# Optimization experiments

Hardware: AMD Instinct MI355X
Metric: run time of the kernel (lower is better)

The kernel has to match this reference:

```python
import jax, jax.numpy as jnp
import numpy as np

B, T, IN_DIM, EMB = 8, 2048, 1024, 1024
NEG_INF = -1e30  # stand-in for float('-inf'); exp() underflows to 0 identically


def setup_inputs() -> dict:
    key = jax.random.key(0)
    ks = jax.random.split(key, 7)
    s = 1.0 / np.sqrt(IN_DIM)
    return {
        "x": jax.random.normal(ks[0], (B, T, IN_DIM), dtype=jnp.float32),
        "Wq": jax.random.normal(ks[1], (IN_DIM, EMB), dtype=jnp.float32) * s,
        "bq": jax.random.normal(ks[2], (EMB,), dtype=jnp.float32) * 0.01,
        "Wk": jax.random.normal(ks[3], (IN_DIM, EMB), dtype=jnp.float32) * s,
        "bk": jax.random.normal(ks[4], (EMB,), dtype=jnp.float32) * 0.01,
        "Wv": jax.random.normal(ks[5], (IN_DIM, EMB), dtype=jnp.float32) * s,
        "bv": jax.random.normal(ks[6], (EMB,), dtype=jnp.float32) * 0.01,
    }


def reference(x, Wq, bq, Wk, bk, Wv, bv):
    # projections: [B, T, EMB]
    q = x @ Wq + bq
    k = x @ Wk + bk
    v = x @ Wv + bv
    scale = jnp.asarray(EMB, x.dtype) ** 0.5
    # scores: [B, T, T]
    scores = jnp.einsum("btd,bsd->bts", q, k) / scale
    Tq = scores.shape[-2]
    causal = jnp.tril(jnp.ones((Tq, Tq), dtype=bool))  # [T, T]
    scores = jnp.where(causal, scores, jnp.asarray(NEG_INF, scores.dtype))
    # Faithful to torch.vmap(softmax): per-batch GLOBAL-matrix softmax
    # (max and sum taken over the whole [T, T] matrix, not per row).
    m = jnp.max(scores, axis=(-2, -1), keepdims=True)
    e = jnp.exp(scores - m)
    w = e / jnp.sum(e, axis=(-2, -1), keepdims=True)
    # output: [B, T, EMB]
    return jnp.einsum("bts,bsd->btd", w, v)
```

## Files before the change

### kernel.cpp

```cpp
#include <hip/hip_runtime.h>
#include <stdint.h>


#define B_   8
#define T_   2048
#define DIM  1024

typedef _Float16 f16;
typedef f16   f16x8 __attribute__((ext_vector_type(8)));
typedef f16   f16x4 __attribute__((ext_vector_type(4)));
typedef float f32x4 __attribute__((ext_vector_type(4)));

typedef const __attribute__((address_space(1))) void gvoid_t;
typedef __attribute__((address_space(3))) void lvoid_t;

__device__ __forceinline__ void stage_half256(const uint16_t* __restrict__ g, int ld,
                                              uint16_t* s, int tid) {
#pragma unroll
  for (int j = 0; j < 2; ++j) {
    int r   = j * 64 + (tid >> 3);
    int seg = (tid & 7) ^ (r & 7);
    const uint16_t* gp = g + (size_t)r * ld + seg * 8;
    uint16_t* sp = s + j * 4096 + (tid >> 6) * 512;
    __builtin_amdgcn_global_load_lds((gvoid_t*)gp, (lvoid_t*)sp, 16, 0, 0);
  }
}

__device__ __forceinline__ f16x8 frag64(const uint16_t* s, int r, int gseg) {
  return *(const f16x8*)(s + r * 64 + ((gseg ^ (r & 7)) * 8));
}

__device__ __forceinline__ void stage_u8k(const uint16_t* __restrict__ g, int ld,
                                          uint16_t* s, int tid) {
  int r   = tid >> 2;
  int seg = (tid & 3) ^ (r & 3);
  const uint16_t* gp = g + (size_t)r * ld + seg * 8;
  uint16_t* sp = s + (tid >> 6) * 512;
  __builtin_amdgcn_global_load_lds((gvoid_t*)gp, (lvoid_t*)sp, 16, 0, 0);
}

__device__ __forceinline__ f16x8 frag32(const uint16_t* s, int r, int gseg) {
  return *(const f16x8*)(s + r * 32 + ((gseg ^ (r & 3)) * 8));
}

__device__ __forceinline__ void lda4(const uint16_t* s, int rbase, int quad, int l15,
                                     f16x8 o[4][2]) {
#pragma unroll
  for (int mf = 0; mf < 4; ++mf) {
    int r = rbase + mf * 16 + l15;
#pragma unroll
    for (int kk = 0; kk < 2; ++kk) o[mf][kk] = frag64(s, r, kk * 4 + quad);
  }
}

__device__ __forceinline__ void ldb1(const uint16_t* s, int rbase, int quad, int l15,
                                     f16x8 o[2]) {
  int r = rbase + l15;
#pragma unroll
  for (int kk = 0; kk < 2; ++kk) o[kk] = frag64(s, r, kk * 4 + quad);
}

__device__ __forceinline__ void lda4q(const uint16_t* s, int rbase, int quad, int l15,
                                      f16x8 o[4]) {
#pragma unroll
  for (int mf = 0; mf < 4; ++mf) o[mf] = frag32(s, rbase + mf * 16 + l15, quad);
}

__device__ __forceinline__ void ldb2q(const uint16_t* s, int rbase, int quad, int l15,
                                      f16x8 o[2]) {
#pragma unroll
  for (int nf = 0; nf < 2; ++nf) o[nf] = frag32(s, rbase + nf * 16 + l15, quad);
}

template <int M0, int N0>
__device__ __forceinline__ void mm8(f16x8 a[4][2], f16x8 b[2], f32x4 (&acc)[8][2]) {
#pragma unroll
  for (int kk = 0; kk < 2; ++kk)
#pragma unroll
    for (int mf = 0; mf < 4; ++mf)
      acc[M0 + mf][N0] = __builtin_amdgcn_mfma_f32_16x16x32_f16(
          a[mf][kk], b[kk], acc[M0 + mf][N0], 0, 0, 0);
}

template <int N0>
__device__ __forceinline__ void mm8q(f16x8 a[4], f16x8 b[2], f32x4 (&acc)[4][4]) {
#pragma unroll
  for (int mf = 0; mf < 4; ++mf)
#pragma unroll
    for (int nf = 0; nf < 2; ++nf)
      acc[mf][N0 + nf] = __builtin_amdgcn_mfma_f32_16x16x32_f16(
          a[mf], b[nf], acc[mf][N0 + nf], 0, 0, 0);
}

#define SYNC_MFMA8(AA, BB, M0, N0)                     \
  __builtin_amdgcn_s_barrier();                        \
  asm volatile("s_waitcnt lgkmcnt(0)" ::: "memory");   \
  __builtin_amdgcn_s_setprio(1);                       \
  mm8<M0, N0>(AA, BB, acc);                            \
  __builtin_amdgcn_s_setprio(0);                       \
  __builtin_amdgcn_s_barrier();

#define SYNC_MFMA8Q(AA, BB, N0)                        \
  __builtin_amdgcn_s_barrier();                        \
  asm volatile("s_waitcnt lgkmcnt(0)" ::: "memory");   \
  __builtin_amdgcn_s_setprio(1);                       \
  mm8q<N0>(AA, BB, acc);                               \
  __builtin_amdgcn_s_setprio(0);                       \
  __builtin_amdgcn_s_barrier();

__device__ __forceinline__ void gemm128x256_bk32(const uint16_t* __restrict__ gA,
                                                 const uint16_t* __restrict__ gB,
                                                 int lda, int ldb, int nTiles,
                                                 uint16_t* smem, f32x4 (&acc)[4][4]) {
  const int tid = threadIdx.x, lane = tid & 63;
  const int quad = lane >> 4, l15 = lane & 15;
  const int wv = tid >> 6, wr = wv >> 2, wc = wv & 3;

  uint16_t* sA0 = smem;
  uint16_t* sA1 = smem + 4096;
  uint16_t* sB0 = smem + 8192;
  uint16_t* sB1 = smem + 16384;

  stage_u8k(gA,                          lda, sA0,        tid);
  stage_u8k(gB,                          ldb, sB0,        tid);
  stage_u8k(gB + 128 * (size_t)ldb,      ldb, sB0 + 4096, tid);
  stage_u8k(gA + 32,                     lda, sA1,        tid);
  asm volatile("s_waitcnt vmcnt(1)" ::: "memory");
  __builtin_amdgcn_s_barrier();

  f16x8 a[4], b0[2], b1[2];
#pragma unroll 1
  for (int it = 0; it < nTiles / 2 - 1; ++it) {
    const uint16_t* gAn = gA + (2 * it + 2) * 32;
    const uint16_t* gBn = gB + (2 * it + 1) * 32;
    lda4q(sA0, wr * 64,      quad, l15, a);
    ldb2q(sB0, wc * 64,      quad, l15, b0);
    stage_u8k(gBn,                     ldb, sB1,        tid);
    stage_u8k(gBn + 128 * (size_t)ldb, ldb, sB1 + 4096, tid);
    SYNC_MFMA8Q(a, b0, 0)
    ldb2q(sB0, wc * 64 + 32, quad, l15, b1);
    stage_u8k(gAn, lda, sA0, tid);
    asm volatile("s_waitcnt vmcnt(1)" ::: "memory");
    SYNC_MFMA8Q(a, b1, 2)
    lda4q(sA1, wr * 64,      quad, l15, a);
    ldb2q(sB1, wc * 64,      quad, l15, b0);
    stage_u8k(gBn + 32,                     ldb, sB0,        tid);
    stage_u8k(gBn + 32 + 128 * (size_t)ldb, ldb, sB0 + 4096, tid);
    SYNC_MFMA8Q(a, b0, 0)
    ldb2q(sB1, wc * 64 + 32, quad, l15, b1);
    stage_u8k(gAn + 32, lda, sA1, tid);
    asm volatile("s_waitcnt vmcnt(1)" ::: "memory");
    SYNC_MFMA8Q(a, b1, 2)
  }
  {
    const uint16_t* gBn = gB + (nTiles - 1) * 32;
    lda4q(sA0, wr * 64,      quad, l15, a);
    ldb2q(sB0, wc * 64,      quad, l15, b0);
    stage_u8k(gBn,                     ldb, sB1,        tid);
    stage_u8k(gBn + 128 * (size_t)ldb, ldb, sB1 + 4096, tid);
    SYNC_MFMA8Q(a, b0, 0)
    ldb2q(sB0, wc * 64 + 32, quad, l15, b1);
    asm volatile("s_waitcnt vmcnt(0)" ::: "memory");
    SYNC_MFMA8Q(a, b1, 2)
    lda4q(sA1, wr * 64,      quad, l15, a);
    ldb2q(sB1, wc * 64,      quad, l15, b0);
    SYNC_MFMA8Q(a, b0, 0)
    ldb2q(sB1, wc * 64 + 32, quad, l15, b1);
    SYNC_MFMA8Q(a, b1, 2)
  }
}

__device__ __forceinline__ void gemm256n128_8ph(const uint16_t* __restrict__ gA,
                                                const uint16_t* __restrict__ gB,
                                                int lda, int ldb, int nIter,
                                                uint16_t* smem, f32x4 (&acc)[8][2]) {
  const int tid = threadIdx.x, lane = tid & 63;
  const int quad = lane >> 4, l15 = lane & 15;
  const int wv = tid >> 6, wr = wv >> 2, wc = wv & 3;

  uint16_t* sA0 = smem;
  uint16_t* sA1 = smem + 16384;
  uint16_t* sB0 = smem + 32768;
  uint16_t* sB1 = smem + 40960;

  stage_half256(gA,                     lda, sA0,        tid);
  stage_half256(gA + 128 * (size_t)lda, lda, sA0 + 8192, tid);
  stage_half256(gB,                     ldb, sB0,        tid);
  stage_half256(gB + 64,                ldb, sB1,        tid);
  asm volatile("s_waitcnt vmcnt(2)" ::: "memory");
  __builtin_amdgcn_s_barrier();

  f16x8 alo[4][2], ahi[4][2], b0[2], b1[2];
#pragma unroll 1
  for (int it = 0; it < nIter - 1; ++it) {
    const int t1 = 2 * it + 1, t2 = 2 * it + 2, t3 = 2 * it + 3;
    const uint16_t* gA1 = gA + t1 * 64;
    const uint16_t* gA2 = gA + t2 * 64;

    lda4(sA0, wr * 128,      quad, l15, alo);
    ldb1(sB0, wc * 32,       quad, l15, b0);
    stage_half256(gA1, lda, sA1, tid);
    SYNC_MFMA8(alo, b0, 0, 0)
    ldb1(sB0, wc * 32 + 16,  quad, l15, b1);
    stage_half256(gA1 + 128 * (size_t)lda, lda, sA1 + 8192, tid);
    SYNC_MFMA8(alo, b1, 0, 1)
    lda4(sA0, wr * 128 + 64, quad, l15, ahi);
    stage_half256(gB + t2 * 64, ldb, sB0, tid);
    SYNC_MFMA8(ahi, b1, 4, 1)
    asm volatile("s_waitcnt vmcnt(2)" ::: "memory");
    SYNC_MFMA8(ahi, b0, 4, 0)
    lda4(sA1, wr * 128,      quad, l15, alo);
    ldb1(sB1, wc * 32,       quad, l15, b0);
    stage_half256(gA2, lda, sA0, tid);
    SYNC_MFMA8(alo, b0, 0, 0)
    ldb1(sB1, wc * 32 + 16,  quad, l15, b1);
    stage_half256(gA2 + 128 * (size_t)lda, lda, sA0 + 8192, tid);
    SYNC_MFMA8(alo, b1, 0, 1)
    lda4(sA1, wr * 128 + 64, quad, l15, ahi);
    stage_half256(gB + t3 * 64, ldb, sB1, tid);
    SYNC_MFMA8(ahi, b1, 4, 1)
    asm volatile("s_waitcnt vmcnt(2)" ::: "memory");
    SYNC_MFMA8(ahi, b0, 4, 0)
  }
  {
    const uint16_t* gA1 = gA + (2 * nIter - 1) * 64;
    lda4(sA0, wr * 128,      quad, l15, alo);
    ldb1(sB0, wc * 32,       quad, l15, b0);
    stage_half256(gA1, lda, sA1, tid);
    SYNC_MFMA8(alo, b0, 0, 0)
    ldb1(sB0, wc * 32 + 16,  quad, l15, b1);
    stage_half256(gA1 + 128 * (size_t)lda, lda, sA1 + 8192, tid);
    SYNC_MFMA8(alo, b1, 0, 1)
    lda4(sA0, wr * 128 + 64, quad, l15, ahi);
    SYNC_MFMA8(ahi, b1, 4, 1)
    asm volatile("s_waitcnt vmcnt(0)" ::: "memory");
    SYNC_MFMA8(ahi, b0, 4, 0)
    lda4(sA1, wr * 128,      quad, l15, alo);
    ldb1(sB1, wc * 32,       quad, l15, b0);
    SYNC_MFMA8(alo, b0, 0, 0)
    ldb1(sB1, wc * 32 + 16,  quad, l15, b1);
    SYNC_MFMA8(alo, b1, 0, 1)
    lda4(sA1, wr * 128 + 64, quad, l15, ahi);
    SYNC_MFMA8(ahi, b1, 4, 1)
    SYNC_MFMA8(ahi, b0, 4, 0)
  }
}


__global__ void zero_lrow_kernel(float* __restrict__ lrow) {
  lrow[blockIdx.x * 256 + threadIdx.x] = 0.f;
}

__global__ void conv_x_kernel(const float* __restrict__ x, f16* __restrict__ xf) {
  size_t i = (size_t)blockIdx.x * 256 + threadIdx.x;
  float4 v = ((const float4*)x)[i];
  f16x4 o = {(f16)v.x, (f16)v.y, (f16)v.z, (f16)v.w};
  ((f16x4*)xf)[i] = o;
}

__global__ void convT_w_kernel(const float* __restrict__ Wq, const float* __restrict__ Wk,
                               const float* __restrict__ Wv, f16* __restrict__ WT) {
  __shared__ float tile[64][65];
  const int z = blockIdx.z;
  const float* W = (z == 0) ? Wq : (z == 1) ? Wk : Wv;
  const int r0 = blockIdx.x * 64, c0 = blockIdx.y * 64, tid = threadIdx.x;
#pragma unroll
  for (int i = 0; i < 16; ++i) {
    int rr = (tid >> 6) + 4 * i, cc = tid & 63;
    tile[rr][cc] = W[(size_t)(r0 + rr) * DIM + c0 + cc];
  }
  __syncthreads();
#pragma unroll
  for (int i = 0; i < 16; ++i) {
    int nn = (tid >> 6) + 4 * i, kk = tid & 63;
    WT[(size_t)z * DIM * DIM + (size_t)(c0 + nn) * DIM + r0 + kk] = (f16)tile[kk][nn];
  }
}

__global__ void reduce_z_kernel(const float* __restrict__ lrow, float* __restrict__ invZ) {
  const int b = blockIdx.x, tid = threadIdx.x;
  float s = 0.f;
  for (int i = tid; i < T_; i += 256) s += lrow[(size_t)b * T_ + i];
#pragma unroll
  for (int off = 1; off < 64; off <<= 1) s += __shfl_xor(s, off, 64);
  __shared__ float red[4];
  if ((tid & 63) == 0) red[tid >> 6] = s;
  __syncthreads();
  if (tid == 0) invZ[b] = 1.0f / (red[0] + red[1] + red[2] + red[3]);
}


__global__ __launch_bounds__(512, 4) void proj_kernel(
    const f16* __restrict__ xf, const f16* __restrict__ WT,
    const float* __restrict__ bq, const float* __restrict__ bk, const float* __restrict__ bv,
    f16* __restrict__ q, f16* __restrict__ k, f16* __restrict__ vT) {
  __shared__ uint16_t smem[24576];

  const int bid = blockIdx.x;
  const int xcd = bid & 7, local = bid >> 3;
  const int bxl = local / 12, zy = local % 12;
  const int bx = xcd * 16 + bxl;
  const int z = zy >> 2, by = zy & 3;
  const size_t arow = (size_t)bx * 128;
  const int    bcol = by * 256;

  f32x4 acc[4][4];
  {
    f32x4 zz = {0.f, 0.f, 0.f, 0.f};
#pragma unroll
    for (int i = 0; i < 4; ++i)
#pragma unroll
      for (int j = 0; j < 4; ++j) acc[i][j] = zz;
  }
  gemm128x256_bk32((const uint16_t*)xf + arow * DIM,
                   (const uint16_t*)WT + (size_t)z * DIM * DIM + (size_t)bcol * DIM,
                   DIM, DIM, 32, smem, acc);

  const float* bias = (z == 0) ? bq : (z == 1) ? bk : bv;
  const int tid = threadIdx.x, lane = tid & 63, wv = tid >> 6;
  const int quad = lane >> 4, l15 = lane & 15;
  const int wr = wv >> 2, wc = wv & 3;
  if (z < 2) {
    f16* O = z ? k : q;
#pragma unroll
    for (int mf = 0; mf < 4; ++mf)
#pragma unroll
      for (int nf = 0; nf < 4; ++nf) {
        int n = bcol + wc * 64 + nf * 16 + l15;
        float bb = bias[n];
        size_t row0 = arow + wr * 64 + mf * 16 + quad * 4;
#pragma unroll
        for (int r = 0; r < 4; ++r)
          O[(row0 + r) * DIM + n] = (f16)(acc[mf][nf][r] + bb);
      }
  } else {
#pragma unroll
    for (int mf = 0; mf < 4; ++mf)
#pragma unroll
      for (int nf = 0; nf < 4; ++nf) {
        int n = bcol + wc * 64 + nf * 16 + l15;
        float bb = bias[n];
        int row0 = (int)arow + wr * 64 + mf * 16 + quad * 4;
        int bb_i = row0 >> 11, t0 = row0 & 2047;
        f16x4 pk;
#pragma unroll
        for (int r = 0; r < 4; ++r) pk[r] = (f16)(acc[mf][nf][r] + bb);
        *(f16x4*)(vT + ((size_t)bb_i * DIM + n) * T_ + t0) = pk;
      }
  }
}

__global__ __launch_bounds__(512, 2) void scores_kernel(
    const f16* __restrict__ q, const f16* __restrict__ k,
    f16* __restrict__ E, float* __restrict__ lrow) {
  __shared__ uint16_t smem[49152];
  const int bid = blockIdx.x;
  const int b = bid & 7, blk = bid >> 3;

  const int tid = threadIdx.x, lane = tid & 63, wv = tid >> 6;
  const int quad = lane >> 4, l15 = lane & 15;
  const int wr = wv >> 2, wc = wv & 3;
  f16*   Eb = E + (size_t)b * T_ * T_;
  float* lb = lrow + (size_t)b * T_;

#pragma unroll 1
  for (int jid = blk; jid < 72; jid += 32) {
    int qi = 0;
    while ((qi + 1) * (qi + 2) <= jid) ++qi;
    const int h = jid - qi * (qi + 1);

    f32x4 acc[8][2];
    {
      f32x4 zz = {0.f, 0.f, 0.f, 0.f};
#pragma unroll
      for (int i = 0; i < 8; ++i) { acc[i][0] = zz; acc[i][1] = zz; }
    }
    gemm256n128_8ph((const uint16_t*)(q + ((size_t)b * T_ + qi * 256) * DIM),
                    (const uint16_t*)(k + ((size_t)b * T_ + h * 128) * DIM),
                    DIM, DIM, 8, smem, acc);

    const bool diag = (h >= 2 * qi);
#pragma unroll
    for (int mf = 0; mf < 8; ++mf) {
      float rs[4] = {0.f, 0.f, 0.f, 0.f};
#pragma unroll
      for (int nf = 0; nf < 2; ++nf)
#pragma unroll
        for (int r = 0; r < 4; ++r) {
          int t = qi * 256 + wr * 128 + mf * 16 + quad * 4 + r;
          int s = h * 128 + wc * 32 + nf * 16 + l15;
          float e = 0.f;
          if (!diag || s <= t) e = __expf(fminf(acc[mf][nf][r] * 0.03125f, 11.f));
          Eb[(size_t)t * T_ + s] = (f16)e;
          rs[r] += e;
        }
#pragma unroll
      for (int off = 1; off < 16; off <<= 1)
#pragma unroll
        for (int r = 0; r < 4; ++r) rs[r] += __shfl_xor(rs[r], off, 64);
      if (l15 == 0)
#pragma unroll
        for (int r = 0; r < 4; ++r)
          atomicAdd(&lb[qi * 256 + wr * 128 + mf * 16 + quad * 4 + r], rs[r]);
    }
  }
}

__global__ __launch_bounds__(512, 2) void pv_kernel(
    const f16* __restrict__ E, const f16* __restrict__ vT,
    const float* __restrict__ invZ, float* __restrict__ out) {
  __shared__ uint16_t smem[49152];
  const int bid = blockIdx.x;
  const int b = bid & 7, local = bid >> 3;
  const int nt = local & 7, pair = local >> 3;

  const float iz = invZ[b];
  const int tid = threadIdx.x, lane = tid & 63, wv = tid >> 6;
  const int quad = lane >> 4, l15 = lane & 15;
  const int wr = wv >> 2, wc = wv & 3;
  float* ob = out + (size_t)b * T_ * DIM;
  const uint16_t* Bv = (const uint16_t*)(vT + ((size_t)b * DIM + nt * 128) * (size_t)T_);

#pragma unroll 1
  for (int j = 0; j < 2; ++j) {
    const int qi = j ? (7 - pair) : pair;
    f32x4 acc[8][2];
    {
      f32x4 z = {0.f, 0.f, 0.f, 0.f};
#pragma unroll
      for (int i = 0; i < 8; ++i) { acc[i][0] = z; acc[i][1] = z; }
    }
    gemm256n128_8ph((const uint16_t*)(E + ((size_t)b * T_ + qi * 256) * (size_t)T_),
                    Bv, T_, T_, (qi + 1) * 2, smem, acc);
#pragma unroll
    for (int mf = 0; mf < 8; ++mf)
#pragma unroll
      for (int nf = 0; nf < 2; ++nf)
#pragma unroll
        for (int r = 0; r < 4; ++r) {
          int t = qi * 256 + wr * 128 + mf * 16 + quad * 4 + r;
          int n = nt * 128 + wc * 32 + nf * 16 + l15;
          ob[(size_t)t * DIM + n] = acc[mf][nf][r] * iz;
        }
  }
}


extern "C" void kernel_launch(void* const* d_in, const int* in_sizes, int n_in,
                              void* d_out, int out_size, void* d_ws, size_t ws_size,
                              hipStream_t stream) {
  const float* x  = (const float*)d_in[0];
  const float* Wq = (const float*)d_in[1];
  const float* bq = (const float*)d_in[2];
  const float* Wk = (const float*)d_in[3];
  const float* bk = (const float*)d_in[4];
  const float* Wv = (const float*)d_in[5];
  const float* bv = (const float*)d_in[6];
  float* out = (float*)d_out;

  char* ws = (char*)d_ws;
  f16*   E    = (f16*)ws;
  f16*   xf   = (f16*)ws;
  f16*   q    = (f16*)(ws + 67108864);
  f16*   k    = (f16*)(ws + 100663296);
  f16*   vT   = (f16*)(ws + 134217728);
  f16*   WT   = (f16*)(ws + 167772160);
  float* lrow = (float*)(ws + 174063616);
  float* invZ = (float*)(ws + 174129152);
  if (ws_size < (size_t)174129184) return;

  zero_lrow_kernel<<<64, 256, 0, stream>>>(lrow);
  conv_x_kernel<<<16384, 256, 0, stream>>>(x, xf);
  convT_w_kernel<<<dim3(16, 16, 3), 256, 0, stream>>>(Wq, Wk, Wv, WT);
  proj_kernel<<<dim3(1536), 512, 0, stream>>>(xf, WT, bq, bk, bv, q, k, vT);
  scores_kernel<<<dim3(256), 512, 0, stream>>>(q, k, E, lrow);
  reduce_z_kernel<<<B_, 256, 0, stream>>>(lrow, invZ);
  pv_kernel<<<dim3(256), 512, 0, stream>>>(E, vT, invZ, out);
}
```

Measured before the change: 366.3 us.

## Retile scores kernel to 128x256 tiles with one tile per block

```diff
diff --git a/kernel.cpp b/kernel.cpp
--- a/kernel.cpp
+++ b/kernel.cpp
@@ -33,14 +33,14 @@
 __device__ __forceinline__ void stage_u8k(const uint16_t* __restrict__ g, int ld,
                                           uint16_t* s, int tid) {
   int r   = tid >> 2;
-  int seg = (tid & 3) ^ (r & 3);
+  int seg = (tid & 3) ^ ((r >> 1) & 3);
   const uint16_t* gp = g + (size_t)r * ld + seg * 8;
   uint16_t* sp = s + (tid >> 6) * 512;
   __builtin_amdgcn_global_load_lds((gvoid_t*)gp, (lvoid_t*)sp, 16, 0, 0);
 }
 
 __device__ __forceinline__ f16x8 frag32(const uint16_t* s, int r, int gseg) {
-  return *(const f16x8*)(s + r * 32 + ((gseg ^ (r & 3)) * 8));
+  return *(const f16x8*)(s + r * 32 + ((gseg ^ ((r >> 1) & 3)) * 8));
 }
 
 __device__ __forceinline__ void lda4(const uint16_t* s, int rbase, int quad, int l15,
@@ -350,59 +350,57 @@
   }
 }
 
-__global__ __launch_bounds__(512, 2) void scores_kernel(
+__global__ __launch_bounds__(512, 4) void scores_kernel(
     const f16* __restrict__ q, const f16* __restrict__ k,
     f16* __restrict__ E, float* __restrict__ lrow) {
-  __shared__ uint16_t smem[49152];
+  __shared__ uint16_t smem[24576];
   const int bid = blockIdx.x;
-  const int b = bid & 7, blk = bid >> 3;
+  const int b = bid & 7;
+  const int jid = bid >> 3;
+  int qs = 0, c = 0;
+  while (c + (qs / 2 + 1) <= jid) { c += qs / 2 + 1; ++qs; }
+  const int kp = jid - c;
+
+  f32x4 acc[4][4];
+  {
+    f32x4 zz = {0.f, 0.f, 0.f, 0.f};
+#pragma unroll
+    for (int i = 0; i < 4; ++i)
+#pragma unroll
+      for (int j = 0; j < 4; ++j) acc[i][j] = zz;
+  }
+  gemm128x256_bk32((const uint16_t*)(q + ((size_t)b * T_ + qs * 128) * DIM),
+                   (const uint16_t*)(k + ((size_t)b * T_ + kp * 256) * DIM),
+                   DIM, DIM, 32, smem, acc);
 
   const int tid = threadIdx.x, lane = tid & 63, wv = tid >> 6;
   const int quad = lane >> 4, l15 = lane & 15;
   const int wr = wv >> 2, wc = wv & 3;
   f16*   Eb = E + (size_t)b * T_ * T_;
   float* lb = lrow + (size_t)b * T_;
-
-#pragma unroll 1
-  for (int jid = blk; jid < 72; jid += 32) {
-    int qi = 0;
-    while ((qi + 1) * (qi + 2) <= jid) ++qi;
-    const int h = jid - qi * (qi + 1);
-
-    f32x4 acc[8][2];
-    {
-      f32x4 zz = {0.f, 0.f, 0.f, 0.f};
-#pragma unroll
-      for (int i = 0; i < 8; ++i) { acc[i][0] = zz; acc[i][1] = zz; }
-    }
-    gemm256n128_8ph((const uint16_t*)(q + ((size_t)b * T_ + qi * 256) * DIM),
-                    (const uint16_t*)(k + ((size_t)b * T_ + h * 128) * DIM),
-                    DIM, DIM, 8, smem, acc);
-
-    const bool diag = (h >= 2 * qi);
-#pragma unroll
-    for (int mf = 0; mf < 8; ++mf) {
-      float rs[4] = {0.f, 0.f, 0.f, 0.f};
-#pragma unroll
-      for (int nf = 0; nf < 2; ++nf)
-#pragma unroll
-        for (int r = 0; r < 4; ++r) {
-          int t = qi * 256 + wr * 128 + mf * 16 + quad * 4 + r;
-          int s = h * 128 + wc * 32 + nf * 16 + l15;
-          float e = 0.f;
-          if (!diag || s <= t) e = __expf(fminf(acc[mf][nf][r] * 0.03125f, 11.f));
-          Eb[(size_t)t * T_ + s] = (f16)e;
-          rs[r] += e;
-        }
-#pragma unroll
-      for (int off = 1; off < 16; off <<= 1)
-#pragma unroll
-        for (int r = 0; r < 4; ++r) rs[r] += __shfl_xor(rs[r], off, 64);
-      if (l15 == 0)
-#pragma unroll
-        for (int r = 0; r < 4; ++r)
-          atomicAdd(&lb[qi * 256 + wr * 128 + mf * 16 + quad * 4 + r], rs[r]);
-    }
+  const bool diag = (qs <= 2 * kp + 1);
+#pragma unroll
+  for (int mf = 0; mf < 4; ++mf) {
+    float rs[4] = {0.f, 0.f, 0.f, 0.f};
+#pragma unroll
+    for (int nf = 0; nf < 4; ++nf)
+#pragma unroll
+      for (int r = 0; r < 4; ++r) {
+        int t = qs * 128 + wr * 64 + mf * 16 + quad * 4 + r;
+        int s = kp * 256 + wc * 64 + nf * 16 + l15;
+        float e = 0.f;
+        if (!diag || s <= t) e = __expf(fminf(acc[mf][nf][r] * 0.03125f, 11.f));
+        Eb[(size_t)t * T_ + s] = (f16)e;
+        rs[r] += e;
+      }
+#pragma unroll
+    for (int off = 1; off < 16; off <<= 1)
+#pragma unroll
+      for (int r = 0; r < 4; ++r) rs[r] += __shfl_xor(rs[r], off, 64);
+    if (l15 == 0)
+#pragma unroll
+      for (int r = 0; r < 4; ++r)
+        atomicAdd(&lb[qs * 128 + wr * 64 + mf * 16 + quad * 4 + r], rs[r]);
   }
 }
 
@@ -473,7 +471,7 @@
   conv_x_kernel<<<16384, 256, 0, stream>>>(x, xf);
   convT_w_kernel<<<dim3(16, 16, 3), 256, 0, stream>>>(Wq, Wk, Wv, WT);
   proj_kernel<<<dim3(1536), 512, 0, stream>>>(xf, WT, bq, bk, bv, q, k, vT);
-  scores_kernel<<<dim3(256), 512, 0, stream>>>(q, k, E, lrow);
+  scores_kernel<<<dim3(576), 512, 0, stream>>>(q, k, E, lrow);
   reduce_z_kernel<<<B_, 256, 0, stream>>>(lrow, invZ);
   pv_kernel<<<dim3(256), 512, 0, stream>>>(E, vT, invZ, out);
 }
```

New measurement: 362.1 us. No clear change (-1.2%).
